# Optimization experiments

Measured on AMD Instinct MI355X. Metric: run time of the kernel, lower is better.

Reference implementation:

```python
import jax, jax.numpy as jnp
import numpy as np

N_USER = 100000
N_ITEM = 100000
N_TAG = 10000
DIM = 128
E_BUYS = 1_000_000
E_REV = 1_000_000
E_TAGS = 1_000_000
W_SCALE = 0.05


def setup_inputs() -> dict:
    key = jax.random.key(0)
    ks = jax.random.split(key, 18)
    inp = {
        "x_user": jax.random.normal(ks[0], (N_USER, DIM), jnp.float32),
        "x_item": jax.random.normal(ks[1], (N_ITEM, DIM), jnp.float32),
        "x_tag": jax.random.normal(ks[2], (N_TAG, DIM), jnp.float32),
        # edge_index per relation: row 0 = src node ids, row 1 = dst node ids
        "ei_buys": jnp.stack([
            jax.random.randint(ks[3], (E_BUYS,), 0, N_USER, jnp.int32),
            jax.random.randint(ks[4], (E_BUYS,), 0, N_ITEM, jnp.int32)]),
        "ei_rev": jnp.stack([
            jax.random.randint(ks[5], (E_REV,), 0, N_ITEM, jnp.int32),
            jax.random.randint(ks[6], (E_REV,), 0, N_USER, jnp.int32)]),
        "ei_tags": jnp.stack([
            jax.random.randint(ks[7], (E_TAGS,), 0, N_TAG, jnp.int32),
            jax.random.randint(ks[8], (E_TAGS,), 0, N_ITEM, jnp.int32)]),
    }
    # SAGEConv params per edge type: lin_l (neighbor agg), lin_r (root), bias
    names = ["buys", "rev", "tags"]
    for i, n in enumerate(names):
        inp[f"Wl_{n}"] = jax.random.normal(ks[9 + 3 * i], (DIM, DIM), jnp.float32) * W_SCALE
        inp[f"Wr_{n}"] = jax.random.normal(ks[10 + 3 * i], (DIM, DIM), jnp.float32) * W_SCALE
        inp[f"b_{n}"] = jnp.zeros((DIM,), jnp.float32)
    return inp


def _sage(x_src, x_dst, ei, Wl, Wr, b):
    """SAGEConv with mean neighbor aggregation: lin_l(mean_j x_j) + lin_r(x_i) + b."""
    n_dst = x_dst.shape[0]
    src, dst = ei[0], ei[1]
    msg_sum = jax.ops.segment_sum(x_src[src], dst, num_segments=n_dst)  # [n_dst, D]
    cnt = jax.ops.segment_sum(jnp.ones(src.shape, x_src.dtype), dst, num_segments=n_dst)
    msg_mean = msg_sum / jnp.maximum(cnt, 1.0)[:, None]
    return msg_mean @ Wl + x_dst @ Wr + b


def reference(x_user, x_item, x_tag, ei_buys, ei_rev, ei_tags,
              Wl_buys, Wr_buys, b_buys,
              Wl_rev, Wr_rev, b_rev,
              Wl_tags, Wr_tags, b_tags):
    # per-relation SAGEConv
    o_item_buys = _sage(x_user, x_item, ei_buys, Wl_buys, Wr_buys, b_buys)
    o_user = _sage(x_item, x_user, ei_rev, Wl_rev, Wr_rev, b_rev)
    o_item_tags = _sage(x_tag, x_item, ei_tags, Wl_tags, Wr_tags, b_tags)
    # HeteroConv aggr='mean' across edge types per destination node type
    out_item = 0.5 * (o_item_buys + o_item_tags)
    out_user = o_user  # single relation into 'user'
    return (out_user, out_item)
```

## Files before the change

### kernel.cpp

```cpp
#include <hip/hip_runtime.h>
#include <hip/hip_bf16.h>
#include <stdint.h>

#define DIM 128
#define NNODE 100000
#define NB 98
#define NBT (3 * NB)
#define T_TILE 8192

typedef __attribute__((ext_vector_type(8))) short short8;
typedef __attribute__((ext_vector_type(4))) float f32x4;

__device__ __forceinline__ unsigned short f32_to_bf16_rne(float f) {
    union { float f; uint32_t u; } v; v.f = f;
    uint32_t u = v.u;
    uint32_t r = u + 0x7FFFu + ((u >> 16) & 1u);
    return (unsigned short)(r >> 16);
}
__device__ __forceinline__ float bf16lo_to_f32(uint32_t u) {
    union { uint32_t i; float f; } v; v.i = u << 16; return v.f;
}
__device__ __forceinline__ float bf16hi_to_f32(uint32_t u) {
    union { uint32_t i; float f; } v; v.i = u & 0xFFFF0000u; return v.f;
}

__global__ void conv_kernel(const float* __restrict__ xu, const float* __restrict__ xi,
                            const float* __restrict__ xt,
                            unsigned short* __restrict__ bu, unsigned short* __restrict__ bi,
                            unsigned short* __restrict__ bt, int nu, int ni, int nt) {
    int idx = blockIdx.x * blockDim.x + threadIdx.x;
    int q_u = nu >> 2, q_i = ni >> 2, q_t = nt >> 2;
    const float* src; unsigned short* dst; int o;
    if (idx < q_u)                { src = xu; dst = bu; o = idx; }
    else if (idx < q_u + q_i)     { src = xi; dst = bi; o = idx - q_u; }
    else if (idx < q_u + q_i+q_t) { src = xt; dst = bt; o = idx - q_u - q_i; }
    else return;
    float4 f = ((const float4*)src)[o];
    ushort4 u;
    u.x = f32_to_bf16_rne(f.x); u.y = f32_to_bf16_rne(f.y);
    u.z = f32_to_bf16_rne(f.z); u.w = f32_to_bf16_rne(f.w);
    ((ushort4*)dst)[o] = u;
}

__global__ __launch_bounds__(256) void coarse_hist(
    const int* __restrict__ ei0, const int* __restrict__ ei1, const int* __restrict__ ei2,
    int E0, int E1, int E2, int* __restrict__ ccnt) {
    __shared__ int h[NBT];
    int Etot = E0 + E1 + E2;
    for (int i = threadIdx.x; i < NBT; i += 256) h[i] = 0;
    __syncthreads();
    for (int e = blockIdx.x * blockDim.x + threadIdx.x; e < Etot; e += gridDim.x * blockDim.x) {
        int rel, le; const int* ei; int E;
        if (e < E0)           { rel = 0; le = e;           ei = ei0; E = E0; }
        else if (e < E0 + E1) { rel = 1; le = e - E0;      ei = ei1; E = E1; }
        else                  { rel = 2; le = e - E0 - E1; ei = ei2; E = E2; }
        int d = ei[E + le];
        atomicAdd(&h[rel * NB + (d >> 10)], 1);
    }
    __syncthreads();
    for (int i = threadIdx.x; i < NBT; i += 256) {
        int c = h[i];
        if (c) atomicAdd(&ccnt[i], c);
    }
}

__global__ void coarse_scan(const int* __restrict__ ccnt, int* __restrict__ bases,
                            int* __restrict__ cursor) {
    if (threadIdx.x == 0) {
        int run = 0;
        for (int i = 0; i < NBT; i++) {
            bases[i] = run; cursor[i] = run;
            run += ccnt[i];
        }
        bases[NBT] = run;
    }
}

__global__ __launch_bounds__(256) void coarse_scatter(
    const int* __restrict__ ei0, const int* __restrict__ ei1, const int* __restrict__ ei2,
    int E0, int E1, int E2, int* __restrict__ cursor, int2* __restrict__ pairs) {
    __shared__ int h[NBT], hb[NBT], lc[NBT];
    int Etot = E0 + E1 + E2;
    int ntiles = (Etot + T_TILE - 1) / T_TILE;
    for (int tile = blockIdx.x; tile < ntiles; tile += gridDim.x) {
        int tbase = tile * T_TILE;
        for (int i = threadIdx.x; i < NBT; i += 256) { h[i] = 0; lc[i] = 0; }
        __syncthreads();
        int dstreg[32], srcreg[32];
        #pragma unroll
        for (int k = 0; k < 32; k++) {
            int e = tbase + k * 256 + threadIdx.x;
            dstreg[k] = -1;
            if (e < Etot) {
                int rel, le; const int* ei; int E;
                if (e < E0)           { rel = 0; le = e;           ei = ei0; E = E0; }
                else if (e < E0 + E1) { rel = 1; le = e - E0;      ei = ei1; E = E1; }
                else                  { rel = 2; le = e - E0 - E1; ei = ei2; E = E2; }
                int d = ei[E + le];
                srcreg[k] = ei[le];
                dstreg[k] = d;
                atomicAdd(&h[rel * NB + (d >> 10)], 1);
            }
        }
        __syncthreads();
        for (int i = threadIdx.x; i < NBT; i += 256) {
            int c = h[i];
            hb[i] = c ? atomicAdd(&cursor[i], c) : 0;
        }
        __syncthreads();
        #pragma unroll
        for (int k = 0; k < 32; k++) {
            int e = tbase + k * 256 + threadIdx.x;
            if (e < Etot) {
                int d = dstreg[k];
                int rel = (e < E0) ? 0 : ((e < E0 + E1) ? 1 : 2);
                int bin = rel * NB + (d >> 10);
                int pos = hb[bin] + atomicAdd(&lc[bin], 1);
                pairs[pos] = make_int2(srcreg[k], d);
            }
        }
        __syncthreads();
    }
}

__global__ __launch_bounds__(256) void fine_sort(
    const int* __restrict__ bases, const int2* __restrict__ pairs,
    int* __restrict__ cnt, int* __restrict__ off, int* __restrict__ sorted, int N) {
    __shared__ int h[1024], ho[1024], ssum[256];
    int b = blockIdx.x;
    int rel = b / NB, jb = b - rel * NB;
    int ebase = bases[b], ne = bases[b + 1] - ebase;
    int dbase = jb << 10;
    int tid = threadIdx.x;
    for (int i = tid; i < 1024; i += 256) h[i] = 0;
    __syncthreads();
    for (int i = tid; i < ne; i += 256) {
        int d = pairs[ebase + i].y;
        atomicAdd(&h[d - dbase], 1);
    }
    __syncthreads();
    int v0 = h[tid * 4], v1 = h[tid * 4 + 1], v2 = h[tid * 4 + 2], v3 = h[tid * 4 + 3];
    int tsum = v0 + v1 + v2 + v3;
    ssum[tid] = tsum;
    __syncthreads();
    for (int s = 1; s < 256; s <<= 1) {
        int t = (tid >= s) ? ssum[tid - s] : 0;
        __syncthreads();
        ssum[tid] += t;
        __syncthreads();
    }
    int excl = ssum[tid] - tsum;
    ho[tid * 4] = excl;
    ho[tid * 4 + 1] = excl + v0;
    ho[tid * 4 + 2] = excl + v0 + v1;
    ho[tid * 4 + 3] = excl + v0 + v1 + v2;
    __syncthreads();
    for (int i = tid; i < 1024; i += 256) {
        int d = dbase + i;
        if (d < N) { cnt[rel * N + d] = h[i]; off[rel * N + d] = ebase + ho[i]; }
        h[i] = 0;
    }
    __syncthreads();
    for (int i = tid; i < ne; i += 256) {
        int2 p = pairs[ebase + i];
        int dl = p.y - dbase;
        int pos = ebase + ho[dl] + atomicAdd(&h[dl], 1);
        sorted[pos] = p.x;
    }
}

__global__ __launch_bounds__(256) void agg_kernel_bf16(
    const unsigned short* __restrict__ xb_user, const unsigned short* __restrict__ xb_item,
    const unsigned short* __restrict__ xb_tag,
    const int* __restrict__ sorted, const int* __restrict__ off,
    const int* __restrict__ cnt, unsigned short* __restrict__ msg, int N) {
    int w = (blockIdx.x * blockDim.x + threadIdx.x) >> 6;
    int lane = threadIdx.x & 63;
    if (w >= 3 * N) return;
    int rel = w / N;
    int d = w - rel * N;
    const unsigned short* xs = (rel == 0) ? xb_user : (rel == 1) ? xb_item : xb_tag;
    int start = off[rel * N + d];
    int deg = cnt[rel * N + d];
    const int* lst = sorted + start;
    int q = lane >> 4;
    int c = lane & 15;
    float a0=0,a1=0,a2=0,a3=0,a4=0,a5=0,a6=0,a7=0;
    #define ACC(U) { \
        a0 += bf16lo_to_f32(U.x); a1 += bf16hi_to_f32(U.x); \
        a2 += bf16lo_to_f32(U.y); a3 += bf16hi_to_f32(U.y); \
        a4 += bf16lo_to_f32(U.z); a5 += bf16hi_to_f32(U.z); \
        a6 += bf16lo_to_f32(U.w); a7 += bf16hi_to_f32(U.w); }
    int i = 0;
    for (; i + 8 <= deg; i += 8) {
        int s0 = lst[i + q];
        int s1 = lst[i + 4 + q];
        uint4 u0 = *(const uint4*)(xs + (size_t)s0 * DIM + c * 8);
        uint4 u1 = *(const uint4*)(xs + (size_t)s1 * DIM + c * 8);
        ACC(u0); ACC(u1);
    }
    int rem = deg - i;
    if (q < rem) {
        int s = lst[i + q];
        uint4 u = *(const uint4*)(xs + (size_t)s * DIM + c * 8);
        ACC(u);
    }
    if (q + 4 < rem) {
        int s = lst[i + 4 + q];
        uint4 u = *(const uint4*)(xs + (size_t)s * DIM + c * 8);
        ACC(u);
    }
    #undef ACC
    a0 += __shfl_xor(a0, 16, 64); a1 += __shfl_xor(a1, 16, 64);
    a2 += __shfl_xor(a2, 16, 64); a3 += __shfl_xor(a3, 16, 64);
    a4 += __shfl_xor(a4, 16, 64); a5 += __shfl_xor(a5, 16, 64);
    a6 += __shfl_xor(a6, 16, 64); a7 += __shfl_xor(a7, 16, 64);
    a0 += __shfl_xor(a0, 32, 64); a1 += __shfl_xor(a1, 32, 64);
    a2 += __shfl_xor(a2, 32, 64); a3 += __shfl_xor(a3, 32, 64);
    a4 += __shfl_xor(a4, 32, 64); a5 += __shfl_xor(a5, 32, 64);
    a6 += __shfl_xor(a6, 32, 64); a7 += __shfl_xor(a7, 32, 64);
    if (q == 0) {
        float inv = 1.0f / (float)max(deg, 1);
        uint4 o;
        o.x = (uint32_t)f32_to_bf16_rne(a0 * inv) | ((uint32_t)f32_to_bf16_rne(a1 * inv) << 16);
        o.y = (uint32_t)f32_to_bf16_rne(a2 * inv) | ((uint32_t)f32_to_bf16_rne(a3 * inv) << 16);
        o.z = (uint32_t)f32_to_bf16_rne(a4 * inv) | ((uint32_t)f32_to_bf16_rne(a5 * inv) << 16);
        o.w = (uint32_t)f32_to_bf16_rne(a6 * inv) | ((uint32_t)f32_to_bf16_rne(a7 * inv) << 16);
        *(uint4*)(msg + (size_t)(rel * N + d) * DIM + c * 8) = o;
    }
}

__global__ void pack_kernel(const float* __restrict__ Wl_b, const float* __restrict__ Wr_b,
                            const float* __restrict__ b_b,
                            const float* __restrict__ Wl_r, const float* __restrict__ Wr_r,
                            const float* __restrict__ b_r,
                            const float* __restrict__ Wl_t, const float* __restrict__ Wr_t,
                            const float* __restrict__ b_t,
                            unsigned short* __restrict__ pw_item,
                            unsigned short* __restrict__ pw_user,
                            float* __restrict__ bias_item, float* __restrict__ bias_user) {
    const int NI = 12 * 8 * 64 * 8;
    const int NU = 8 * 8 * 64 * 8;
    int o = blockIdx.x * blockDim.x + threadIdx.x;
    if (o < NI) {
        int j = o & 7, lane = (o >> 3) & 63, ks = o >> 12;
        int n = ((o >> 9) & 7) * 16 + (lane & 15);
        int k = (ks & 3) * 32 + (lane >> 4) * 8 + j;
        int src = ks >> 2;
        float v;
        if (src == 0)      v = 0.5f * Wl_b[k * DIM + n];
        else if (src == 1) v = 0.5f * Wl_t[k * DIM + n];
        else               v = 0.5f * (Wr_b[k * DIM + n] + Wr_t[k * DIM + n]);
        pw_item[o] = f32_to_bf16_rne(v);
    } else if (o < NI + NU) {
        int oo = o - NI;
        int j = oo & 7, lane = (oo >> 3) & 63, ks = oo >> 12;
        int n = ((oo >> 9) & 7) * 16 + (lane & 15);
        int k = (ks & 3) * 32 + (lane >> 4) * 8 + j;
        float v = ((ks >> 2) == 0) ? Wl_r[k * DIM + n] : Wr_r[k * DIM + n];
        pw_user[oo] = f32_to_bf16_rne(v);
    } else {
        int oo = o - NI - NU;
        if (oo < DIM)            bias_item[oo] = 0.5f * (b_b[oo] + b_t[oo]);
        else if (oo < 2 * DIM)   bias_user[oo - DIM] = b_r[oo - DIM];
    }
}

__global__ __launch_bounds__(256) void gemm_kernel(
    const unsigned short* __restrict__ Abf0,
    const unsigned short* __restrict__ Abf1,
    const unsigned short* __restrict__ Abf2,
    int n_src,
    const unsigned short* __restrict__ packW,
    const float* __restrict__ bias,
    float* __restrict__ out, int M) {
    int wave = threadIdx.x >> 6;
    int lane = threadIdx.x & 63;
    int quad = lane >> 4;
    int l15  = lane & 15;
    int m0   = blockIdx.x * 64 + wave * 16;
    int arow = m0 + l15;
    bool arow_ok = arow < M;
    int nks = n_src * 4;

    f32x4 acc[8];
    #pragma unroll
    for (int i = 0; i < 8; i++) acc[i] = (f32x4){0.f, 0.f, 0.f, 0.f};

    for (int ks = 0; ks < nks; ks++) {
        int src = ks >> 2;
        int kofs = (ks & 3) * 32 + quad * 8;
        short8 afrag;
        const unsigned short* A = (src == 0) ? Abf0 : (src == 1) ? Abf1 : Abf2;
        if (arow_ok) afrag = *(const short8*)(A + (size_t)arow * DIM + kofs);
        else         afrag = (short8){0,0,0,0,0,0,0,0};
        const unsigned short* wp = packW + ((size_t)ks * 8 * 64 + lane) * 8;
        #pragma unroll
        for (int nt = 0; nt < 8; nt++) {
            short8 wfrag = *(const short8*)(wp + (size_t)nt * 64 * 8);
            acc[nt] = __builtin_amdgcn_mfma_f32_16x16x32_bf16(afrag, wfrag, acc[nt], 0, 0, 0);
        }
    }
    #pragma unroll
    for (int nt = 0; nt < 8; nt++) {
        int col = nt * 16 + l15;
        float bv = bias[col];
        #pragma unroll
        for (int r = 0; r < 4; r++) {
            int row = m0 + quad * 4 + r;
            if (row < M) out[(size_t)row * DIM + col] = acc[nt][r] + bv;
        }
    }
}

extern "C" void kernel_launch(void* const* d_in, const int* in_sizes, int n_in,
                              void* d_out, int out_size, void* d_ws, size_t ws_size,
                              hipStream_t stream) {
    const float* x_user = (const float*)d_in[0];
    const float* x_item = (const float*)d_in[1];
    const float* x_tag  = (const float*)d_in[2];
    const int* ei_buys  = (const int*)d_in[3];
    const int* ei_rev   = (const int*)d_in[4];
    const int* ei_tags  = (const int*)d_in[5];
    const float* Wl_b = (const float*)d_in[6];
    const float* Wr_b = (const float*)d_in[7];
    const float* b_b  = (const float*)d_in[8];
    const float* Wl_r = (const float*)d_in[9];
    const float* Wr_r = (const float*)d_in[10];
    const float* b_r  = (const float*)d_in[11];
    const float* Wl_t = (const float*)d_in[12];
    const float* Wr_t = (const float*)d_in[13];
    const float* b_t  = (const float*)d_in[14];

    const int N  = NNODE;
    const int E0 = in_sizes[3] / 2, E1 = in_sizes[4] / 2, E2 = in_sizes[5] / 2;
    const int n_user = in_sizes[0], n_item = in_sizes[1], n_tag = in_sizes[2];

    char* w = (char*)d_ws;
    int* cnt    = (int*)(w + 0);
    int* off    = (int*)(w + 1200000);
    int* ccnt   = (int*)(w + 2400000);
    int* bases  = (int*)(w + 2401280);
    int* cursor = (int*)(w + 2402560);
    int* sorted = (int*)(w + 2403840);
    unsigned short* msg = (unsigned short*)(w + 15600000);
    int2* pairs = (int2*)(w + 15600000);
    unsigned short* pw_item = (unsigned short*)(w + 92400000);
    unsigned short* pw_user = (unsigned short*)(w + 92498304);
    float* bias_item = (float*)(w + 92563840);
    float* bias_user = (float*)(w + 92564352);
    unsigned short* xb_user = (unsigned short*)(w + 92564992);
    unsigned short* xb_item = (unsigned short*)(w + 118164992);
    unsigned short* xb_tag  = (unsigned short*)(w + 143764992);

    float* out_user = (float*)d_out;
    float* out_item = out_user + (size_t)N * DIM;

    int Etot = E0 + E1 + E2;

    hipMemsetAsync(ccnt, 0, NBT * sizeof(int), stream);

    pack_kernel<<<(49152 + 32768 + 2 * DIM + 255) / 256, 256, 0, stream>>>(
        Wl_b, Wr_b, b_b, Wl_r, Wr_r, b_r, Wl_t, Wr_t, b_t,
        pw_item, pw_user, bias_item, bias_user);

    int tot4 = (n_user + n_item + n_tag) / 4;
    conv_kernel<<<(tot4 + 255) / 256, 256, 0, stream>>>(
        x_user, x_item, x_tag, xb_user, xb_item, xb_tag, n_user, n_item, n_tag);

    coarse_hist<<<512, 256, 0, stream>>>(ei_buys, ei_rev, ei_tags, E0, E1, E2, ccnt);

    coarse_scan<<<1, 64, 0, stream>>>(ccnt, bases, cursor);

    int ntiles = (Etot + T_TILE - 1) / T_TILE;
    coarse_scatter<<<ntiles, 256, 0, stream>>>(
        ei_buys, ei_rev, ei_tags, E0, E1, E2, cursor, pairs);

    fine_sort<<<NBT, 256, 0, stream>>>(bases, pairs, cnt, off, sorted, N);

    agg_kernel_bf16<<<(3 * N * 64 + 255) / 256, 256, 0, stream>>>(
        xb_user, xb_item, xb_tag, sorted, off, cnt, msg, N);

    gemm_kernel<<<(N + 63) / 64, 256, 0, stream>>>(
        msg, msg + 2 * (size_t)N * DIM, xb_item, 3, pw_item, bias_item, out_item, N);

    gemm_kernel<<<(N + 63) / 64, 256, 0, stream>>>(
        msg + (size_t)N * DIM, xb_user, nullptr, 2, pw_user, bias_user, out_user, N);
}
```

Measured before the change: 513.5 us.

## Pack sort pairs into 32-bit words, derive degree from offsets, half-wave aggregation

The coarse scatter now stores each edge as one 32-bit word: the source id in 17 bits and the local destination offset within its 1024-node bin in the upper bits. This halves the pair traffic through the scatter and the fine sort. The separate count array is dropped, and the aggregation kernel computes each node's degree from consecutive offsets, which relies on offsets being contiguous across relations. Aggregation now gives each destination node a half-wave, with each lane loading 8 bytes per neighbor and a 4-way unrolled sequential loop. This removes the cross-lane shuffle reduction but gives up the parallel fetch of several neighbors per node.

```diff
diff --git a/kernel.cpp b/kernel.cpp
--- a/kernel.cpp
+++ b/kernel.cpp
@@ -78,7 +78,7 @@
 
 __global__ __launch_bounds__(256) void coarse_scatter(
     const int* __restrict__ ei0, const int* __restrict__ ei1, const int* __restrict__ ei2,
-    int E0, int E1, int E2, int* __restrict__ cursor, int2* __restrict__ pairs) {
+    int E0, int E1, int E2, int* __restrict__ cursor, int* __restrict__ pairs) {
     __shared__ int h[NBT], hb[NBT], lc[NBT];
     int Etot = E0 + E1 + E2;
     int ntiles = (Etot + T_TILE - 1) / T_TILE;
@@ -86,20 +86,22 @@
         int tbase = tile * T_TILE;
         for (int i = threadIdx.x; i < NBT; i += 256) { h[i] = 0; lc[i] = 0; }
         __syncthreads();
-        int dstreg[32], srcreg[32];
+        int binreg[32], valreg[32];
         #pragma unroll
         for (int k = 0; k < 32; k++) {
             int e = tbase + k * 256 + threadIdx.x;
-            dstreg[k] = -1;
+            binreg[k] = -1;
             if (e < Etot) {
                 int rel, le; const int* ei; int E;
                 if (e < E0)           { rel = 0; le = e;           ei = ei0; E = E0; }
                 else if (e < E0 + E1) { rel = 1; le = e - E0;      ei = ei1; E = E1; }
                 else                  { rel = 2; le = e - E0 - E1; ei = ei2; E = E2; }
                 int d = ei[E + le];
-                srcreg[k] = ei[le];
-                dstreg[k] = d;
-                atomicAdd(&h[rel * NB + (d >> 10)], 1);
+                int s = ei[le];
+                int bin = rel * NB + (d >> 10);
+                binreg[k] = bin;
+                valreg[k] = s | ((d & 1023) << 17);
+                atomicAdd(&h[bin], 1);
             }
         }
         __syncthreads();
@@ -110,13 +112,10 @@
         __syncthreads();
         #pragma unroll
         for (int k = 0; k < 32; k++) {
-            int e = tbase + k * 256 + threadIdx.x;
-            if (e < Etot) {
-                int d = dstreg[k];
-                int rel = (e < E0) ? 0 : ((e < E0 + E1) ? 1 : 2);
-                int bin = rel * NB + (d >> 10);
+            if (binreg[k] >= 0) {
+                int bin = binreg[k];
                 int pos = hb[bin] + atomicAdd(&lc[bin], 1);
-                pairs[pos] = make_int2(srcreg[k], d);
+                pairs[pos] = valreg[k];
             }
         }
         __syncthreads();
@@ -124,8 +123,8 @@
 }
 
 __global__ __launch_bounds__(256) void fine_sort(
-    const int* __restrict__ bases, const int2* __restrict__ pairs,
-    int* __restrict__ cnt, int* __restrict__ off, int* __restrict__ sorted, int N) {
+    const int* __restrict__ bases, const int* __restrict__ pairs,
+    int* __restrict__ off, int* __restrict__ sorted, int N) {
     __shared__ int h[1024], ho[1024], ssum[256];
     int b = blockIdx.x;
     int rel = b / NB, jb = b - rel * NB;
@@ -135,8 +134,8 @@
     for (int i = tid; i < 1024; i += 256) h[i] = 0;
     __syncthreads();
     for (int i = tid; i < ne; i += 256) {
-        int d = pairs[ebase + i].y;
-        atomicAdd(&h[d - dbase], 1);
+        int dl = pairs[ebase + i] >> 17;
+        atomicAdd(&h[dl], 1);
     }
     __syncthreads();
     int v0 = h[tid * 4], v1 = h[tid * 4 + 1], v2 = h[tid * 4 + 2], v3 = h[tid * 4 + 3];
@@ -157,15 +156,15 @@
     __syncthreads();
     for (int i = tid; i < 1024; i += 256) {
         int d = dbase + i;
-        if (d < N) { cnt[rel * N + d] = h[i]; off[rel * N + d] = ebase + ho[i]; }
+        if (d < N) off[rel * N + d] = ebase + ho[i];
         h[i] = 0;
     }
     __syncthreads();
     for (int i = tid; i < ne; i += 256) {
-        int2 p = pairs[ebase + i];
-        int dl = p.y - dbase;
+        int p = pairs[ebase + i];
+        int dl = p >> 17;
         int pos = ebase + ho[dl] + atomicAdd(&h[dl], 1);
-        sorted[pos] = p.x;
+        sorted[pos] = p & 0x1FFFF;
     }
 }
 
@@ -173,61 +172,46 @@
     const unsigned short* __restrict__ xb_user, const unsigned short* __restrict__ xb_item,
     const unsigned short* __restrict__ xb_tag,
     const int* __restrict__ sorted, const int* __restrict__ off,
-    const int* __restrict__ cnt, unsigned short* __restrict__ msg, int N) {
+    unsigned short* __restrict__ msg, int N, int Etot) {
     int w = (blockIdx.x * blockDim.x + threadIdx.x) >> 6;
     int lane = threadIdx.x & 63;
-    if (w >= 3 * N) return;
-    int rel = w / N;
-    int d = w - rel * N;
+    int hh = lane >> 5;
+    int c = lane & 31;
+    int g = w * 2 + hh;
+    if (g >= 3 * N) return;
+    int rel = g / N;
     const unsigned short* xs = (rel == 0) ? xb_user : (rel == 1) ? xb_item : xb_tag;
-    int start = off[rel * N + d];
-    int deg = cnt[rel * N + d];
-    const int* lst = sorted + start;
-    int q = lane >> 4;
-    int c = lane & 15;
-    float a0=0,a1=0,a2=0,a3=0,a4=0,a5=0,a6=0,a7=0;
-    #define ACC(U) { \
-        a0 += bf16lo_to_f32(U.x); a1 += bf16hi_to_f32(U.x); \
-        a2 += bf16lo_to_f32(U.y); a3 += bf16hi_to_f32(U.y); \
-        a4 += bf16lo_to_f32(U.z); a5 += bf16hi_to_f32(U.z); \
-        a6 += bf16lo_to_f32(U.w); a7 += bf16hi_to_f32(U.w); }
+    int o0 = off[g];
+    int o1 = (g + 1 < 3 * N) ? off[g + 1] : Etot;
+    int deg = o1 - o0;
+    const int* lst = sorted + o0;
+    int c4 = c * 4;
+    f32x4 a0 = (f32x4){0,0,0,0}, a1 = (f32x4){0,0,0,0};
+    f32x4 a2 = (f32x4){0,0,0,0}, a3 = (f32x4){0,0,0,0};
+    #define ACCUM(A, U) { \
+        A[0] += bf16lo_to_f32(U.x); A[1] += bf16hi_to_f32(U.x); \
+        A[2] += bf16lo_to_f32(U.y); A[3] += bf16hi_to_f32(U.y); }
     int i = 0;
-    for (; i + 8 <= deg; i += 8) {
-        int s0 = lst[i + q];
-        int s1 = lst[i + 4 + q];
-        uint4 u0 = *(const uint4*)(xs + (size_t)s0 * DIM + c * 8);
-        uint4 u1 = *(const uint4*)(xs + (size_t)s1 * DIM + c * 8);
-        ACC(u0); ACC(u1);
-    }
-    int rem = deg - i;
-    if (q < rem) {
-        int s = lst[i + q];
-        uint4 u = *(const uint4*)(xs + (size_t)s * DIM + c * 8);
-        ACC(u);
-    }
-    if (q + 4 < rem) {
-        int s = lst[i + 4 + q];
-        uint4 u = *(const uint4*)(xs + (size_t)s * DIM + c * 8);
-        ACC(u);
-    }
-    #undef ACC
-    a0 += __shfl_xor(a0, 16, 64); a1 += __shfl_xor(a1, 16, 64);
-    a2 += __shfl_xor(a2, 16, 64); a3 += __shfl_xor(a3, 16, 64);
-    a4 += __shfl_xor(a4, 16, 64); a5 += __shfl_xor(a5, 16, 64);
-    a6 += __shfl_xor(a6, 16, 64); a7 += __shfl_xor(a7, 16, 64);
-    a0 += __shfl_xor(a0, 32, 64); a1 += __shfl_xor(a1, 32, 64);
-    a2 += __shfl_xor(a2, 32, 64); a3 += __shfl_xor(a3, 32, 64);
-    a4 += __shfl_xor(a4, 32, 64); a5 += __shfl_xor(a5, 32, 64);
-    a6 += __shfl_xor(a6, 32, 64); a7 += __shfl_xor(a7, 32, 64);
-    if (q == 0) {
-        float inv = 1.0f / (float)max(deg, 1);
-        uint4 o;
-        o.x = (uint32_t)f32_to_bf16_rne(a0 * inv) | ((uint32_t)f32_to_bf16_rne(a1 * inv) << 16);
-        o.y = (uint32_t)f32_to_bf16_rne(a2 * inv) | ((uint32_t)f32_to_bf16_rne(a3 * inv) << 16);
-        o.z = (uint32_t)f32_to_bf16_rne(a4 * inv) | ((uint32_t)f32_to_bf16_rne(a5 * inv) << 16);
-        o.w = (uint32_t)f32_to_bf16_rne(a6 * inv) | ((uint32_t)f32_to_bf16_rne(a7 * inv) << 16);
-        *(uint4*)(msg + (size_t)(rel * N + d) * DIM + c * 8) = o;
-    }
+    for (; i + 4 <= deg; i += 4) {
+        int s0 = lst[i], s1 = lst[i + 1], s2 = lst[i + 2], s3 = lst[i + 3];
+        uint2 u0 = *(const uint2*)(xs + (size_t)s0 * DIM + c4);
+        uint2 u1 = *(const uint2*)(xs + (size_t)s1 * DIM + c4);
+        uint2 u2 = *(const uint2*)(xs + (size_t)s2 * DIM + c4);
+        uint2 u3 = *(const uint2*)(xs + (size_t)s3 * DIM + c4);
+        ACCUM(a0, u0); ACCUM(a1, u1); ACCUM(a2, u2); ACCUM(a3, u3);
+    }
+    for (; i < deg; i++) {
+        int s0 = lst[i];
+        uint2 u0 = *(const uint2*)(xs + (size_t)s0 * DIM + c4);
+        ACCUM(a0, u0);
+    }
+    #undef ACCUM
+    f32x4 s = (a0 + a1) + (a2 + a3);
+    float inv = 1.0f / (float)max(deg, 1);
+    uint2 o;
+    o.x = (uint32_t)f32_to_bf16_rne(s[0] * inv) | ((uint32_t)f32_to_bf16_rne(s[1] * inv) << 16);
+    o.y = (uint32_t)f32_to_bf16_rne(s[2] * inv) | ((uint32_t)f32_to_bf16_rne(s[3] * inv) << 16);
+    *(uint2*)(msg + (size_t)g * DIM + c4) = o;
 }
 
 __global__ void pack_kernel(const float* __restrict__ Wl_b, const float* __restrict__ Wr_b,
@@ -337,14 +321,13 @@
     const int n_user = in_sizes[0], n_item = in_sizes[1], n_tag = in_sizes[2];
 
     char* w = (char*)d_ws;
-    int* cnt    = (int*)(w + 0);
     int* off    = (int*)(w + 1200000);
     int* ccnt   = (int*)(w + 2400000);
     int* bases  = (int*)(w + 2401280);
     int* cursor = (int*)(w + 2402560);
     int* sorted = (int*)(w + 2403840);
     unsigned short* msg = (unsigned short*)(w + 15600000);
-    int2* pairs = (int2*)(w + 15600000);
+    int* pairs  = (int*)(w + 15600000);
     unsigned short* pw_item = (unsigned short*)(w + 92400000);
     unsigned short* pw_user = (unsigned short*)(w + 92498304);
     float* bias_item = (float*)(w + 92563840);
@@ -376,10 +359,11 @@
     coarse_scatter<<<ntiles, 256, 0, stream>>>(
         ei_buys, ei_rev, ei_tags, E0, E1, E2, cursor, pairs);
 
-    fine_sort<<<NBT, 256, 0, stream>>>(bases, pairs, cnt, off, sorted, N);
-
-    agg_kernel_bf16<<<(3 * N * 64 + 255) / 256, 256, 0, stream>>>(
-        xb_user, xb_item, xb_tag, sorted, off, cnt, msg, N);
+    fine_sort<<<NBT, 256, 0, stream>>>(bases, pairs, off, sorted, N);
+
+    int nwaves = (3 * N + 1) / 2;
+    agg_kernel_bf16<<<(nwaves * 64 + 255) / 256, 256, 0, stream>>>(
+        xb_user, xb_item, xb_tag, sorted, off, msg, N, Etot);
 
     gemm_kernel<<<(N + 63) / 64, 256, 0, stream>>>(
         msg, msg + 2 * (size_t)N * DIM, xb_item, 3, pw_item, bias_item, out_item, N);
```

New measurement: 504.7 us. No clear change (-1.7%).
